# Kernel tuning notes

Hardware: AMD Instinct MI355X
Metric: run time of the kernel (lower is better)

The kernel has to match this reference:

```python
import jax, jax.numpy as jnp
import numpy as np

N, D_IN, D_OUT = 1024, 512, 128
DROP_P = 0.4


def setup_inputs() -> dict:
    key = jax.random.key(0)
    k1, k2, k3, k4, kw, kb = jax.random.split(key, 6)
    inp = {
        "x1": jax.random.normal(k1, (N, D_IN), dtype=jnp.float32),
        "x2": jax.random.normal(k2, (N, D_IN), dtype=jnp.float32),
        "x3": jax.random.normal(k3, (N, D_IN), dtype=jnp.float32),
        "x4": jax.random.normal(k4, (N, D_IN), dtype=jnp.float32),
        # Linear(D_IN, D_OUT): torch stores weight as [out, in]
        "W": jax.random.normal(kw, (D_OUT, D_IN), dtype=jnp.float32) * (1.0 / np.sqrt(D_IN)),
        "b": jax.random.normal(kb, (D_OUT,), dtype=jnp.float32) * 0.01,
    }
    return inp


def reference(x1, x2, x3, x4, W, b):
    lin = lambda x: x @ W.T + b            # shared Linear, [N, D_OUT]
    q = lin(x1)
    k = lin(x2)
    v = lin(x3)
    scale = lin(x4)                         # [N, D]
    # softmax over dim=0 (across rows), then unsqueeze(-1) -> [N, D, 1]
    inv_scale = jax.nn.softmax(scale, axis=0)[..., None]
    qk = q @ k.T                            # [N, N]
    # broadcast divide: [N,1,N] / [N,D,1] -> [N, D, N]
    scaled_qk = qk[:, None, :] / inv_scale
    softmax_qk = jax.nn.softmax(scaled_qk, axis=-1)
    # dropout p=0.4 (training mode), deterministic key for reproducibility
    keep = jax.random.bernoulli(jax.random.key(42), 1.0 - DROP_P, softmax_qk.shape)
    dropout_qk = jnp.where(keep, softmax_qk / (1.0 - DROP_P), 0.0)
    # torch broadcast matmul: [N,D,N] @ [N,D] -> [N,D,D]
    output = jnp.einsum('ndm,mk->ndk', dropout_qk, v)
    return output
```

## Files before the change

### kernel.cpp

```cpp
#include <hip/hip_runtime.h>
#include <stdint.h>
#include <math.h>

static constexpr int NN  = 1024;
static constexpr int DIN = 512;
static constexpr int DD  = 128;

__device__ __forceinline__ uint32_t rotl32(uint32_t x, uint32_t r) {
  return (x << r) | (x >> (32u - r));
}

__device__ __forceinline__ bool keep_mask(uint32_t idx) {
  uint32_t x0 = 0u, x1 = idx;
  const uint32_t k0 = 0u, k1 = 42u;
  const uint32_t k2 = k0 ^ k1 ^ 0x1BD11BDAu;
  x0 += k0; x1 += k1;
#define TF_ROUND(r) { x0 += x1; x1 = rotl32(x1, r); x1 ^= x0; }
  TF_ROUND(13u) TF_ROUND(15u) TF_ROUND(26u) TF_ROUND(6u)
  x0 += k1; x1 += k2 + 1u;
  TF_ROUND(17u) TF_ROUND(29u) TF_ROUND(16u) TF_ROUND(24u)
  x0 += k2; x1 += k0 + 2u;
  TF_ROUND(13u) TF_ROUND(15u) TF_ROUND(26u) TF_ROUND(6u)
  x0 += k0; x1 += k1 + 3u;
  TF_ROUND(17u) TF_ROUND(29u) TF_ROUND(16u) TF_ROUND(24u)
  x0 += k1; x1 += k2 + 4u;
  TF_ROUND(13u) TF_ROUND(15u) TF_ROUND(26u) TF_ROUND(6u)
  x0 += k2; x1 += k0 + 5u;
#undef TF_ROUND
  const uint32_t bits = x0 ^ x1;
  const float u = __uint_as_float((bits >> 9) | 0x3f800000u) - 1.0f;
  return u < 0.6f;
}

__global__ __launch_bounds__(256) void lin_kernel(
    const float* __restrict__ x1, const float* __restrict__ x2,
    const float* __restrict__ x3, const float* __restrict__ x4,
    const float* __restrict__ W, const float* __restrict__ bias,
    float* __restrict__ q, float* __restrict__ kk,
    float* __restrict__ v, float* __restrict__ sc) {
  __shared__ float Ws[128 * 66];
  __shared__ float Xs[8 * 68];
  const int t = threadIdx.x;
  const int n0 = blockIdx.x * 8;
  const int mat = blockIdx.y;
  const float* x = (mat == 0) ? x1 : (mat == 1) ? x2 : (mat == 2) ? x3 : x4;
  float* o = (mat == 0) ? q : (mat == 1) ? kk : (mat == 2) ? v : sc;
  const int tx = t & 31;
  const int ty = t >> 5;
  float acc[4] = {0.f, 0.f, 0.f, 0.f};
  for (int kt = 0; kt < 8; ++kt) {
    const int k0 = kt * 64;
    __syncthreads();
    for (int it = 0; it < 8; ++it) {
      const int i = t + 256 * it;
      const int r = i >> 4, c = (i & 15) * 4;
      const float4 wv = *(const float4*)&W[r * DIN + k0 + c];
      *(float2*)&Ws[r * 66 + c]     = make_float2(wv.x, wv.y);
      *(float2*)&Ws[r * 66 + c + 2] = make_float2(wv.z, wv.w);
    }
    if (t < 128) {
      const int r = t >> 4, c = (t & 15) * 4;
      *(float4*)&Xs[r * 68 + c] = *(const float4*)&x[(n0 + r) * DIN + k0 + c];
    }
    __syncthreads();
    for (int c4 = 0; c4 < 64; c4 += 4) {
      const float4 xa = *(const float4*)&Xs[ty * 68 + c4];
#pragma unroll
      for (int j = 0; j < 4; ++j) {
        const float2 w0 = *(const float2*)&Ws[(tx + 32 * j) * 66 + c4];
        const float2 w1 = *(const float2*)&Ws[(tx + 32 * j) * 66 + c4 + 2];
        acc[j] = fmaf(xa.x, w0.x, fmaf(xa.y, w0.y, fmaf(xa.z, w1.x, fmaf(xa.w, w1.y, acc[j]))));
      }
    }
  }
#pragma unroll
  for (int j = 0; j < 4; ++j) {
    const int d = tx + 32 * j;
    o[(n0 + ty) * DD + d] = acc[j] + bias[d];
  }
}

__global__ __launch_bounds__(256) void mid_kernel(
    const float* __restrict__ q, const float* __restrict__ kref,
    const float* __restrict__ sc, float* __restrict__ qkout,
    float* __restrict__ inv) {
  const int t = threadIdx.x;
  if (blockIdx.x < 256) {
    __shared__ float qs[64 * 132];
    __shared__ float ks[64 * 132];
    const int tx = t & 15, ty = t >> 4;
    const int tm = (blockIdx.x & 15) * 64, tn = (blockIdx.x >> 4) * 64;
    for (int it = 0; it < 8; ++it) {
      const int i = t + 256 * it;
      const int r = i >> 5, c = (i & 31) * 4;
      *(float4*)&qs[r * 132 + c] = *(const float4*)&q[(tn + r) * DD + c];
      *(float4*)&ks[r * 132 + c] = *(const float4*)&kref[(tm + r) * DD + c];
    }
    __syncthreads();
    float acc[4][4] = {};
    for (int k0 = 0; k0 < DD; k0 += 4) {
      float4 qv[4], kv[4];
#pragma unroll
      for (int i = 0; i < 4; ++i) qv[i] = *(const float4*)&qs[(ty * 4 + i) * 132 + k0];
#pragma unroll
      for (int j = 0; j < 4; ++j) kv[j] = *(const float4*)&ks[(tx + 16 * j) * 132 + k0];
#pragma unroll
      for (int i = 0; i < 4; ++i)
#pragma unroll
        for (int j = 0; j < 4; ++j)
          acc[i][j] = fmaf(qv[i].x, kv[j].x,
                      fmaf(qv[i].y, kv[j].y,
                      fmaf(qv[i].z, kv[j].z,
                      fmaf(qv[i].w, kv[j].w, acc[i][j]))));
    }
#pragma unroll
    for (int i = 0; i < 4; ++i)
#pragma unroll
      for (int j = 0; j < 4; ++j)
        qkout[(size_t)(tn + ty * 4 + i) * NN + tm + tx + 16 * j] = acc[i][j];
  } else {
    __shared__ float red[256];
    const int d = blockIdx.x - 256;
    float vals[4];
    float mx = -INFINITY;
#pragma unroll
    for (int i = 0; i < 4; ++i) {
      vals[i] = sc[(size_t)(t + 256 * i) * DD + d];
      mx = fmaxf(mx, vals[i]);
    }
    red[t] = mx; __syncthreads();
    for (int s = 128; s > 0; s >>= 1) {
      if (t < s) red[t] = fmaxf(red[t], red[t + s]);
      __syncthreads();
    }
    mx = red[0]; __syncthreads();
    float e[4]; float sm = 0.f;
#pragma unroll
    for (int i = 0; i < 4; ++i) { e[i] = expf(vals[i] - mx); sm += e[i]; }
    red[t] = sm; __syncthreads();
    for (int s = 128; s > 0; s >>= 1) {
      if (t < s) red[t] += red[t + s];
      __syncthreads();
    }
    sm = red[0];
#pragma unroll
    for (int i = 0; i < 4; ++i)
      inv[(size_t)(t + 256 * i) * DD + d] = e[i] / sm;
  }
}

__global__ __launch_bounds__(256) void attn_kernel(
    const float* __restrict__ qk, const float* __restrict__ inv_scale,
    const float* __restrict__ v, float* __restrict__ out) {
  __shared__ float qkrow[NN];
  __shared__ float red[8];
  __shared__ int   surv[NN];
  __shared__ float Pl[16][130];
  __shared__ float Vs[16][132];
  __shared__ float sdv[DD];
  __shared__ float rsl[DD];
  __shared__ int   cnt;

  const int n = blockIdx.x;
  const int t = threadIdx.x;

  const float4 q4 = *(const float4*)&qk[(size_t)n * NN + t * 4];
  *(float4*)&qkrow[t * 4] = q4;
  float mx = fmaxf(fmaxf(q4.x, q4.y), fmaxf(q4.z, q4.w));
#pragma unroll
  for (int o = 32; o > 0; o >>= 1) mx = fmaxf(mx, __shfl_xor(mx, o));
  if ((t & 63) == 0) red[t >> 6] = mx;
  float iv = 0.f;
  if (t < DD) { iv = inv_scale[n * DD + t]; sdv[t] = 1.0f / iv; }
  float miv = iv;
#pragma unroll
  for (int o = 32; o > 0; o >>= 1) miv = fmaxf(miv, __shfl_xor(miv, o));
  if ((t & 63) == 0) red[4 + (t >> 6)] = miv;
  if (t == 0) cnt = 0;
  __syncthreads();
  const float qkmax = fmaxf(fmaxf(red[0], red[1]), fmaxf(red[2], red[3]));
  const float maxinv = fmaxf(red[4], red[5]);
  const float th = qkmax - 30.f * maxinv;

  {
    const float qv[4] = {q4.x, q4.y, q4.z, q4.w};
#pragma unroll
    for (int j = 0; j < 4; ++j)
      if (qv[j] > th) { const int p = atomicAdd(&cnt, 1); surv[p] = t * 4 + j; }
  }
  __syncthreads();
  const int K = cnt;

  const int k4 = (t & 31) * 4;
  const int dbase = t >> 5;
  float4 acc4[16];
#pragma unroll
  for (int g = 0; g < 16; ++g) acc4[g] = make_float4(0.f, 0.f, 0.f, 0.f);
  float Sloc = 0.f;

  for (int c0 = 0; c0 < K; c0 += 16) {
    const int C = min(16, K - c0);
    __syncthreads();
    if (t < DD) {
      const float sd = sdv[t];
      const uint32_t dg = ((uint32_t)(n * DD + t)) << 10;
      for (int s = 0; s < C; ++s) {
        const int m = surv[c0 + s];
        const float arg = (qkrow[m] - qkmax) * sd;
        const float e = __expf(arg);
        Sloc += e;
        float p = 0.f;
        if (arg > -30.f) {
          if (keep_mask(dg + (uint32_t)m)) p = e;
        }
        Pl[s][t] = p;
      }
    } else {
      const int u = t - 128;
      for (int slot = u; slot < C * 32; slot += 128) {
        const int s = slot >> 5, c = (slot & 31) * 4;
        *(float4*)&Vs[s][c] = *(const float4*)&v[(size_t)surv[c0 + s] * DD + c];
      }
    }
    __syncthreads();
    for (int s = 0; s < C; ++s) {
      const float4 vv = *(const float4*)&Vs[s][k4];
#pragma unroll
      for (int g = 0; g < 16; ++g) {
        const float p = Pl[s][g * 8 + dbase];
        acc4[g].x = fmaf(p, vv.x, acc4[g].x);
        acc4[g].y = fmaf(p, vv.y, acc4[g].y);
        acc4[g].z = fmaf(p, vv.z, acc4[g].z);
        acc4[g].w = fmaf(p, vv.w, acc4[g].w);
      }
    }
  }

  __syncthreads();
  if (t < DD) rsl[t] = 1.0f / (Sloc * 0.6f);
  __syncthreads();
  float* op = &out[(size_t)n * (DD * DD) + t * 4];
#pragma unroll
  for (int g = 0; g < 16; ++g) {
    const float rs = rsl[g * 8 + dbase];
    float4 r = acc4[g];
    r.x *= rs; r.y *= rs; r.z *= rs; r.w *= rs;
    *(float4*)&op[g * 1024] = r;
  }
}

extern "C" void kernel_launch(void* const* d_in, const int* in_sizes, int n_in,
                              void* d_out, int out_size, void* d_ws, size_t ws_size,
                              hipStream_t stream) {
  const float* x1 = (const float*)d_in[0];
  const float* x2 = (const float*)d_in[1];
  const float* x3 = (const float*)d_in[2];
  const float* x4 = (const float*)d_in[3];
  const float* W  = (const float*)d_in[4];
  const float* b  = (const float*)d_in[5];
  float* out = (float*)d_out;

  float* ws  = (float*)d_ws;
  float* q   = ws;
  float* k   = ws + 131072;
  float* v   = ws + 262144;
  float* sc  = ws + 393216;
  float* inv = ws + 524288;
  float* qkm = ws + 655360;

  lin_kernel<<<dim3(128, 4), 256, 0, stream>>>(x1, x2, x3, x4, W, b, q, k, v, sc);
  mid_kernel<<<dim3(384), 256, 0, stream>>>(q, k, sc, qkm, inv);
  attn_kernel<<<NN, 256, 0, stream>>>(qkm, inv, v, out);
}
```

Measured before the change: 126.7 us.

## Pre-transpose W into interleaved layout and stream it from global in linear kernel

Adds a small kernel that rewrites W into a k4-major layout with four consecutive k values per output column. The linear kernel then loads all eight input rows into shared memory once and reads W directly from global/L2 as coalesced float4 loads, with no per-tile W staging or repeated barriers. This aims to cut shared-memory traffic and synchronisation in the projection stage. The cost is one extra kernel launch plus workspace traffic, and W is now re-read from cache by every block.

```diff
diff --git a/kernel.cpp b/kernel.cpp
--- a/kernel.cpp
+++ b/kernel.cpp
@@ -32,52 +32,56 @@
   return u < 0.6f;
 }
 
+__global__ __launch_bounds__(256) void wtrans_kernel(
+    const float* __restrict__ W, float* __restrict__ WTp) {
+  const int t = threadIdx.x;
+  const int d = blockIdx.x * 2 + (t >> 7);
+  const int k4 = t & 127;
+  const float4 w = *(const float4*)&W[d * DIN + k4 * 4];
+  *(float4*)&WTp[(size_t)k4 * (DD * 4) + d * 4] = w;
+}
+
 __global__ __launch_bounds__(256) void lin_kernel(
     const float* __restrict__ x1, const float* __restrict__ x2,
     const float* __restrict__ x3, const float* __restrict__ x4,
-    const float* __restrict__ W, const float* __restrict__ bias,
+    const float* __restrict__ WTp, const float* __restrict__ bias,
     float* __restrict__ q, float* __restrict__ kk,
     float* __restrict__ v, float* __restrict__ sc) {
-  __shared__ float Ws[128 * 66];
-  __shared__ float Xs[8 * 68];
+  __shared__ float Xs[8 * 516];
   const int t = threadIdx.x;
   const int n0 = blockIdx.x * 8;
   const int mat = blockIdx.y;
   const float* x = (mat == 0) ? x1 : (mat == 1) ? x2 : (mat == 2) ? x3 : x4;
   float* o = (mat == 0) ? q : (mat == 1) ? kk : (mat == 2) ? v : sc;
-  const int tx = t & 31;
-  const int ty = t >> 5;
+
+#pragma unroll
+  for (int it = 0; it < 4; ++it) {
+    const int i = t + 256 * it;
+    const int r = i >> 7, c = (i & 127) * 4;
+    *(float4*)&Xs[r * 516 + c] = *(const float4*)&x[(size_t)(n0 + r) * DIN + c];
+  }
+  __syncthreads();
+
+  const int d = t & 127;
+  const int g2 = t >> 7;
   float acc[4] = {0.f, 0.f, 0.f, 0.f};
-  for (int kt = 0; kt < 8; ++kt) {
-    const int k0 = kt * 64;
-    __syncthreads();
-    for (int it = 0; it < 8; ++it) {
-      const int i = t + 256 * it;
-      const int r = i >> 4, c = (i & 15) * 4;
-      const float4 wv = *(const float4*)&W[r * DIN + k0 + c];
-      *(float2*)&Ws[r * 66 + c]     = make_float2(wv.x, wv.y);
-      *(float2*)&Ws[r * 66 + c + 2] = make_float2(wv.z, wv.w);
-    }
-    if (t < 128) {
-      const int r = t >> 4, c = (t & 15) * 4;
-      *(float4*)&Xs[r * 68 + c] = *(const float4*)&x[(n0 + r) * DIN + k0 + c];
-    }
-    __syncthreads();
-    for (int c4 = 0; c4 < 64; c4 += 4) {
-      const float4 xa = *(const float4*)&Xs[ty * 68 + c4];
-#pragma unroll
-      for (int j = 0; j < 4; ++j) {
-        const float2 w0 = *(const float2*)&Ws[(tx + 32 * j) * 66 + c4];
-        const float2 w1 = *(const float2*)&Ws[(tx + 32 * j) * 66 + c4 + 2];
-        acc[j] = fmaf(xa.x, w0.x, fmaf(xa.y, w0.y, fmaf(xa.z, w1.x, fmaf(xa.w, w1.y, acc[j]))));
-      }
-    }
-  }
-#pragma unroll
-  for (int j = 0; j < 4; ++j) {
-    const int d = tx + 32 * j;
-    o[(n0 + ty) * DD + d] = acc[j] + bias[d];
-  }
+  const float* wp = &WTp[d * 4];
+
+#pragma unroll 4
+  for (int k4 = 0; k4 < 128; ++k4) {
+    const float4 w4 = *(const float4*)&wp[(size_t)k4 * (DD * 4)];
+#pragma unroll
+    for (int j = 0; j < 4; ++j) {
+      const float4 xa = *(const float4*)&Xs[(g2 * 4 + j) * 516 + k4 * 4];
+      acc[j] = fmaf(xa.x, w4.x, fmaf(xa.y, w4.y,
+               fmaf(xa.z, w4.z, fmaf(xa.w, w4.w, acc[j]))));
+    }
+  }
+
+  const float bd = bias[d];
+#pragma unroll
+  for (int j = 0; j < 4; ++j)
+    o[(size_t)(n0 + g2 * 4 + j) * DD + d] = acc[j] + bd;
 }
 
 __global__ __launch_bounds__(256) void mid_kernel(
@@ -260,15 +264,17 @@
   const float* b  = (const float*)d_in[5];
   float* out = (float*)d_out;
 
-  float* ws  = (float*)d_ws;
-  float* q   = ws;
-  float* k   = ws + 131072;
-  float* v   = ws + 262144;
-  float* sc  = ws + 393216;
-  float* inv = ws + 524288;
-  float* qkm = ws + 655360;
-
-  lin_kernel<<<dim3(128, 4), 256, 0, stream>>>(x1, x2, x3, x4, W, b, q, k, v, sc);
+  float* ws   = (float*)d_ws;
+  float* q    = ws;
+  float* k    = ws + 131072;
+  float* v    = ws + 262144;
+  float* sc   = ws + 393216;
+  float* inv  = ws + 524288;
+  float* qkm  = ws + 655360;
+  float* WTp  = ws + 1703936;
+
+  wtrans_kernel<<<dim3(64), 256, 0, stream>>>(W, WTp);
+  lin_kernel<<<dim3(128, 4), 256, 0, stream>>>(x1, x2, x3, x4, WTp, b, q, k, v, sc);
   mid_kernel<<<dim3(384), 256, 0, stream>>>(q, k, sc, qkm, inv);
   attn_kernel<<<NN, 256, 0, stream>>>(qkm, inv, v, out);
 }
```

New measurement: 118.6 us. 1.07x faster.
